# Performance work log

Measured on AMD Instinct MI355X. Metric: run time of the kernel, lower is better.

## Reference

```python
import jax, jax.numpy as jnp
import numpy as np

D_MODEL = 768
N_HEADS = 12
D_K = D_MODEL // N_HEADS
B, S = 4, 2048


def setup_inputs() -> dict:
    key = jax.random.key(0)
    ks = jax.random.split(key, 9)
    sc = 1.0 / np.sqrt(D_MODEL)
    return {
        "query": jax.random.normal(ks[0], (B, S, D_MODEL), jnp.float32),
        "key": jax.random.normal(ks[1], (B, S, D_MODEL), jnp.float32),
        "value": jax.random.normal(ks[2], (B, S, D_MODEL), jnp.float32),
        "W_Q": jax.random.normal(ks[3], (D_MODEL, D_MODEL), jnp.float32) * sc,
        "b_Q": jax.random.normal(ks[4], (D_MODEL,), jnp.float32) * sc,
        "W_K": jax.random.normal(ks[5], (D_MODEL, D_MODEL), jnp.float32) * sc,
        "b_K": jax.random.normal(ks[6], (D_MODEL,), jnp.float32) * sc,
        "W_V": jax.random.normal(ks[7], (D_MODEL, D_MODEL), jnp.float32) * sc,
        "b_V": jax.random.normal(ks[8], (D_MODEL,), jnp.float32) * sc,
    }


def reference(query, key, value, W_Q, b_Q, W_K, b_K, W_V, b_V):
    b = query.shape[0]
    # QKV projections -> [B, H, S, d_k]
    def split_heads(x):
        return x.reshape(b, -1, N_HEADS, D_K).transpose(0, 2, 1, 3)
    q = split_heads(query @ W_Q + b_Q)
    k = split_heads(key @ W_K + b_K)
    v = split_heads(value @ W_V + b_V)
    # scores [B, H, Sq, Sk]
    scores = jnp.einsum("bhqd,bhkd->bhqk", q, k) / np.sqrt(D_K).astype(jnp.float32)
    attn = jax.nn.softmax(scores, axis=-1)
    ctx = jnp.einsum("bhqk,bhkd->bhqd", attn, v)
    # merge heads -> [B, S, d_model]; note: original forward does NOT apply self.linear
    return ctx.transpose(0, 2, 1, 3).reshape(b, -1, N_HEADS * D_K)
```

## Files before the change

### kernel.cpp

```cpp
#include <hip/hip_runtime.h>
#include <math.h>

#define D_MODEL 768
#define NH      12
#define DK      64
#define BATCH   4
#define SEQ     2048
#define QSCALE  0.18033688011112042f
#define MFIX    10.0f

typedef _Float16 v8h __attribute__((ext_vector_type(8)));
typedef _Float16 v4h __attribute__((ext_vector_type(4)));
typedef float    v4f __attribute__((ext_vector_type(4)));
typedef int      v4i __attribute__((ext_vector_type(4)));

#define MFMA16(a, b, c) __builtin_amdgcn_mfma_f32_16x16x32_f16(a, b, c, 0, 0, 0)

__device__ __forceinline__ void async16(const void* g, void* l) {
    __builtin_amdgcn_global_load_lds(
        (const __attribute__((address_space(1))) unsigned int*)g,
        (__attribute__((address_space(3))) unsigned int*)l, 16, 0, 0);
}

#define WH_PER_Z   589824
#define XH_PER_Z   6291456
#define BH_HALVES  131072

__global__ __launch_bounds__(256) void prep_kernel(
    const float* __restrict__ q_in, const float* __restrict__ k_in,
    const float* __restrict__ v_in,
    const float* __restrict__ Wq, const float* __restrict__ Wk,
    const float* __restrict__ Wv,
    _Float16* __restrict__ Xh, _Float16* __restrict__ Wh)
{
    const int kt = blockIdx.x, my = blockIdx.y, z = blockIdx.z;
    const int t = threadIdx.x;
    __shared__ __align__(16) char smraw[32 * 132 * 4];

    if (my < 64) {
        const int mt = my;
        _Float16* Ah = (_Float16*)smraw;
        const float* X = (z == 0) ? q_in : (z == 1) ? k_in : v_in;
        _Float16* dst = Xh + (((size_t)z * 64 + mt) * 24 + kt) * 4096;
        #pragma unroll
        for (int i = 0; i < 4; i++) {
            int f = t + i * 256;
            int m = f >> 3, kq = (f & 7) * 4;
            float4 xv = *(const float4*)&X[((size_t)mt * 128 + m) * D_MODEL +
                                           kt * 32 + kq];
            auto p0 = __builtin_amdgcn_cvt_pkrtz(xv.x, xv.y);
            auto p1 = __builtin_amdgcn_cvt_pkrtz(xv.z, xv.w);
            v4h hv; hv[0] = p0[0]; hv[1] = p0[1]; hv[2] = p1[0]; hv[3] = p1[1];
            *(v4h*)&Ah[((m >> 4) * 64 + (m & 15) + 16 * (kq >> 3)) * 8 + (kq & 7)] = hv;
        }
        __syncthreads();
        #pragma unroll
        for (int it = 0; it < 2; it++) {
            int c = t + it * 256;
            *(v8h*)&dst[c * 8] = *(v8h*)&Ah[c * 8];
        }
    } else {
        float (*Wl)[132] = (float(*)[132])smraw;
        const float* W = (z == 0) ? Wq : (z == 1) ? Wk : Wv;
        const int mtx = my - 64;
        for (int nn = 0; nn < 3; nn++) {
            const int nt = mtx * 3 + nn;
            _Float16* dst = Wh + ((size_t)z * 144 + nt * 24 + kt) * 4096;
            #pragma unroll
            for (int i = 0; i < 4; i++) {
                int f = t + i * 256;
                int r = f >> 5, c4 = (f & 31) * 4;
                *(float4*)&Wl[r][c4] =
                    *(const float4*)&W[(size_t)(kt * 32 + r) * D_MODEL +
                                       nt * 128 + c4];
            }
            __syncthreads();
            #pragma unroll
            for (int it = 0; it < 2; it++) {
                int c = t + it * 256;
                int nsub = c >> 6, cl = c & 63;
                int n = nsub * 16 + (cl & 15);
                int k = (cl >> 4) * 8;
                v8h hv;
                #pragma unroll
                for (int j = 0; j < 8; j++) hv[j] = (_Float16)Wl[k + j][n];
                *(v8h*)&dst[c * 8] = hv;
            }
            __syncthreads();
        }
    }
}

__global__ __launch_bounds__(256) void proj_kernel(
    const _Float16* __restrict__ Xh, const _Float16* __restrict__ Wh,
    const float* __restrict__ bq, const float* __restrict__ bk,
    const float* __restrict__ bv,
    _Float16* __restrict__ Qs, _Float16* __restrict__ Ks,
    _Float16* __restrict__ Vs)
{
    const int d  = blockIdx.x + 6 * (blockIdx.y + 64 * blockIdx.z);
    const int cx = d & 7, jj = d >> 3;
    const int g  = cx + 8 * (jj / 6);
    const int l  = g * 6 + (jj % 6);
    const int nt = l % 6;
    const int mz = l / 6;
    const int mt = mz & 63;
    const int z  = mz >> 6;

    const float* bias = (z == 0) ? bq : (z == 1) ? bk : bv;
    const _Float16* Xz = Xh + ((size_t)z * 64 + mt) * 24 * 4096;
    const _Float16* Wz = Wh + ((size_t)z * 144 + nt * 24) * 4096;

    const int t = threadIdx.x;
    const int lane = t & 63, w = t >> 6;
    const int wm = w & 1, wn = w >> 1;
    const int l15 = lane & 15, quad = lane >> 4;

    __shared__ _Float16 C[128 * 136];

    const _Float16* Abase = Xz + wm * 2048 + lane * 8;
    const _Float16* Bbase = Wz + wn * 2048 + lane * 8;

    v4f acc[4][4];
    #pragma unroll
    for (int i = 0; i < 4; i++)
        #pragma unroll
        for (int j = 0; j < 4; j++) acc[i][j] = (v4f){0.f, 0.f, 0.f, 0.f};

    v8h a[4], b[4];
    #pragma unroll
    for (int i = 0; i < 4; i++) a[i] = *(const v8h*)(Abase + i * 512);
    #pragma unroll
    for (int j = 0; j < 4; j++) b[j] = *(const v8h*)(Bbase + j * 512);

    #pragma unroll 4
    for (int kt = 0; kt < 24; kt++) {
        v8h an[4], bn[4];
        if (kt < 23) {
            const _Float16* An = Abase + (size_t)(kt + 1) * 4096;
            const _Float16* Bn = Bbase + (size_t)(kt + 1) * 4096;
            #pragma unroll
            for (int i = 0; i < 4; i++) an[i] = *(const v8h*)(An + i * 512);
            #pragma unroll
            for (int j = 0; j < 4; j++) bn[j] = *(const v8h*)(Bn + j * 512);
        }
        #pragma unroll
        for (int i = 0; i < 4; i++)
            #pragma unroll
            for (int j = 0; j < 4; j++)
                acc[i][j] = MFMA16(a[i], b[j], acc[i][j]);
        #pragma unroll
        for (int i = 0; i < 4; i++) { a[i] = an[i]; b[i] = bn[i]; }
    }

    if (z < 2) {
        #pragma unroll
        for (int i = 0; i < 4; i++) {
            #pragma unroll
            for (int j = 0; j < 4; j++) {
                float bval = bias[nt * 128 + wn * 64 + j * 16 + l15];
                #pragma unroll
                for (int r = 0; r < 4; r++) {
                    float val = acc[i][j][r] + bval;
                    if (z == 0) val *= QSCALE;
                    C[(wm * 64 + i * 16 + quad * 4 + r) * 136 +
                      wn * 64 + j * 16 + l15] = (_Float16)val;
                }
            }
        }
    } else {
        #pragma unroll
        for (int i = 0; i < 4; i++) {
            #pragma unroll
            for (int j = 0; j < 4; j++) {
                float bval = bias[nt * 128 + wn * 64 + j * 16 + l15];
                v4h hv;
                #pragma unroll
                for (int r = 0; r < 4; r++) hv[r] = (_Float16)(acc[i][j][r] + bval);
                *(v4h*)&C[(wn * 64 + j * 16 + l15) * 136 +
                          wm * 64 + i * 16 + quad * 4] = hv;
            }
        }
    }
    __syncthreads();

    const int bb = mt >> 4;
    if (z < 2) {
        _Float16* dstT = (z == 0) ? Qs : Ks;
        #pragma unroll
        for (int it = 0; it < 8; it++) {
            int c = t + it * 256;
            int hh = c >> 10, cl = c & 1023;
            int qsub = cl >> 7, rest = cl & 127;
            int dt = rest >> 6, cc = rest & 63;
            v8h val = *(v8h*)&C[(qsub * 16 + (cc & 15)) * 136 +
                                hh * 64 + dt * 32 + (cc >> 4) * 8];
            int h = nt * 2 + hh;
            int qt = (mt & 15) * 8 + qsub;
            *(v8h*)&dstT[(size_t)(bb * NH + h) * BH_HALVES +
                         ((qt * 2 + dt) * 64 + cc) * 8] = val;
        }
    } else {
        #pragma unroll
        for (int it = 0; it < 8; it++) {
            int c = t + it * 256;
            int hh = c >> 10, cl = c & 1023;
            int j32s = cl >> 8, rest = cl & 255;
            int dt16 = rest >> 6, cc = rest & 63;
            int gg = cc >> 4, d15 = cc & 15;
            const _Float16* bp =
                &C[(hh * 64 + dt16 * 16 + d15) * 136 + j32s * 32 + gg * 4];
            v4h lo = *(const v4h*)bp;
            v4h hi = *(const v4h*)(bp + 16);
            v8h val;
            val[0] = lo[0]; val[1] = lo[1]; val[2] = lo[2]; val[3] = lo[3];
            val[4] = hi[0]; val[5] = hi[1]; val[6] = hi[2]; val[7] = hi[3];
            int h = nt * 2 + hh;
            int j32g = (mt & 15) * 4 + j32s;
            *(v8h*)&Vs[(size_t)(bb * NH + h) * BH_HALVES +
                       ((j32g * 4 + dt16) * 64 + cc) * 8] = val;
        }
    }
}

__global__ __launch_bounds__(256) void attn_kernel(
    const _Float16* __restrict__ Qs, const _Float16* __restrict__ Ks,
    const _Float16* __restrict__ Vs, float* __restrict__ out)
{
    const int qb = blockIdx.x, h = blockIdx.y, b = blockIdx.z;
    const int t = threadIdx.x;
    const int lane = t & 63, w = t >> 6;
    const int l15 = lane & 15, quad = lane >> 4;
    const size_t bh = (size_t)(b * NH + h);
    const _Float16* Qb = Qs + bh * BH_HALVES;
    const _Float16* Kb = Ks + bh * BH_HALVES;
    const _Float16* Vb = Vs + bh * BH_HALVES;

    __shared__ _Float16 smem[16384];
    _Float16* Kbuf = smem;
    _Float16* Vbuf = smem + 8192;

    v8h qf[2][2];
    #pragma unroll
    for (int i = 0; i < 2; i++)
        #pragma unroll
        for (int dk = 0; dk < 2; dk++) {
            int qt = qb * 8 + w * 2 + i;
            qf[i][dk] = *(const v8h*)&Qb[((qt * 2 + dk) * 64 + lane) * 8];
        }

    v8h ones;
    #pragma unroll
    for (int j = 0; j < 8; j++) ones[j] = (_Float16)1.0f;

    v4f o[2][4];
    v4f osum[2];
    #pragma unroll
    for (int i = 0; i < 2; i++) {
        osum[i] = (v4f){0.f, 0.f, 0.f, 0.f};
        #pragma unroll
        for (int dt = 0; dt < 4; dt++) o[i][dt] = (v4f){0.f, 0.f, 0.f, 0.f};
    }

    auto chunk_compute = [&](const _Float16* Kl, const _Float16* Vl) {
        v4f sc[2][4];
        #pragma unroll
        for (int i = 0; i < 2; i++)
            #pragma unroll
            for (int nt = 0; nt < 4; nt++)
                sc[i][nt] = (v4f){-MFIX, -MFIX, -MFIX, -MFIX};
        __builtin_amdgcn_s_setprio(1);
        #pragma unroll
        for (int nt = 0; nt < 4; nt++) {
            #pragma unroll
            for (int dk = 0; dk < 2; dk++) {
                v8h kf = *(v8h*)&Kl[((nt * 2 + dk) * 64 + lane) * 8];
                sc[0][nt] = MFMA16(kf, qf[0][dk], sc[0][nt]);
                sc[1][nt] = MFMA16(kf, qf[1][dk], sc[1][nt]);
            }
        }
        __builtin_amdgcn_s_setprio(0);

        v4i paw[2][2];
        #pragma unroll
        for (int i = 0; i < 2; i++) {
            #pragma unroll
            for (int nt = 0; nt < 4; nt++) {
                float p0 = __builtin_amdgcn_exp2f(sc[i][nt][0]);
                float p1 = __builtin_amdgcn_exp2f(sc[i][nt][1]);
                float p2 = __builtin_amdgcn_exp2f(sc[i][nt][2]);
                float p3 = __builtin_amdgcn_exp2f(sc[i][nt][3]);
                auto h0 = __builtin_amdgcn_cvt_pkrtz(p0, p1);
                auto h1 = __builtin_amdgcn_cvt_pkrtz(p2, p3);
                paw[i][nt >> 1][(nt & 1) * 2 + 0] = __builtin_bit_cast(int, h0);
                paw[i][nt >> 1][(nt & 1) * 2 + 1] = __builtin_bit_cast(int, h1);
            }
        }

        __builtin_amdgcn_s_setprio(1);
        #pragma unroll
        for (int mf = 0; mf < 2; mf++) {
            v8h pa0 = __builtin_bit_cast(v8h, paw[0][mf]);
            v8h pa1 = __builtin_bit_cast(v8h, paw[1][mf]);
            #pragma unroll
            for (int dt = 0; dt < 4; dt++) {
                v8h vf = *(v8h*)&Vl[((mf * 4 + dt) * 64 + lane) * 8];
                o[0][dt] = MFMA16(pa0, vf, o[0][dt]);
                o[1][dt] = MFMA16(pa1, vf, o[1][dt]);
            }
            osum[0] = MFMA16(pa0, ones, osum[0]);
            osum[1] = MFMA16(pa1, ones, osum[1]);
        }
        __builtin_amdgcn_s_setprio(0);
    };

    async16(Kb + (size_t)t * 8,         Kbuf + t * 8);
    async16(Kb + (size_t)(t + 256) * 8, Kbuf + (t + 256) * 8);
    async16(Vb + (size_t)t * 8,         Vbuf + t * 8);
    async16(Vb + (size_t)(t + 256) * 8, Vbuf + (t + 256) * 8);

    for (int c = 0; c < 32; c += 2) {
        asm volatile("s_waitcnt vmcnt(0)" ::: "memory");
        __syncthreads();
        {
            const _Float16* ks = Kb + (size_t)(c + 1) * 4096;
            const _Float16* vs = Vb + (size_t)(c + 1) * 4096;
            async16(ks + (size_t)t * 8,         Kbuf + 4096 + t * 8);
            async16(ks + (size_t)(t + 256) * 8, Kbuf + 4096 + (t + 256) * 8);
            async16(vs + (size_t)t * 8,         Vbuf + 4096 + t * 8);
            async16(vs + (size_t)(t + 256) * 8, Vbuf + 4096 + (t + 256) * 8);
        }
        chunk_compute(Kbuf, Vbuf);

        asm volatile("s_waitcnt vmcnt(0)" ::: "memory");
        __syncthreads();
        if (c < 30) {
            const _Float16* ks = Kb + (size_t)(c + 2) * 4096;
            const _Float16* vs = Vb + (size_t)(c + 2) * 4096;
            async16(ks + (size_t)t * 8,         Kbuf + t * 8);
            async16(ks + (size_t)(t + 256) * 8, Kbuf + (t + 256) * 8);
            async16(vs + (size_t)t * 8,         Vbuf + t * 8);
            async16(vs + (size_t)(t + 256) * 8, Vbuf + (t + 256) * 8);
        }
        chunk_compute(Kbuf + 4096, Vbuf + 4096);
    }

    #pragma unroll
    for (int i = 0; i < 2; i++) {
        #pragma unroll
        for (int r = 0; r < 4; r++) {
            float inv = 1.0f / osum[i][r];
            int s = qb * 128 + w * 32 + i * 16 + quad * 4 + r;
            #pragma unroll
            for (int dt = 0; dt < 4; dt++)
                out[((size_t)b * SEQ + s) * D_MODEL + h * DK + dt * 16 + l15] =
                    o[i][dt][r] * inv;
        }
    }
}

extern "C" void kernel_launch(void* const* d_in, const int* in_sizes, int n_in,
                              void* d_out, int out_size, void* d_ws, size_t ws_size,
                              hipStream_t stream)
{
    const float* q_in = (const float*)d_in[0];
    const float* k_in = (const float*)d_in[1];
    const float* v_in = (const float*)d_in[2];
    const float* Wq   = (const float*)d_in[3];
    const float* bq   = (const float*)d_in[4];
    const float* Wk   = (const float*)d_in[5];
    const float* bk   = (const float*)d_in[6];
    const float* Wv   = (const float*)d_in[7];
    const float* bv   = (const float*)d_in[8];
    float* out = (float*)d_out;

    _Float16* Wh = (_Float16*)d_ws;
    _Float16* Xh = Wh + 3 * (size_t)WH_PER_Z;
    _Float16* Qs = Xh + 3 * (size_t)XH_PER_Z;
    _Float16* Ks = Qs + (size_t)BATCH * NH * BH_HALVES;
    _Float16* Vs = Ks + (size_t)BATCH * NH * BH_HALVES;

    prep_kernel<<<dim3(24, 66, 3), 256, 0, stream>>>(q_in, k_in, v_in,
                                                     Wq, Wk, Wv, Xh, Wh);
    proj_kernel<<<dim3(6, 64, 3), 256, 0, stream>>>(Xh, Wh, bq, bk, bv,
                                                    Qs, Ks, Vs);
    attn_kernel<<<dim3(16, NH, BATCH), 256, 0, stream>>>(Qs, Ks, Vs, out);
}
```

Before: 240.3 us.

## Fuse fp32-to-fp16 activation conversion into projection GEMM, drop Xh staging

The projection kernel now reads the fp32 query/key/value activations directly and converts them to fp16 in registers right before the MFMAs. The prep pass that wrote a pre-swizzled fp16 copy of the activations is gone, leaving a small kernel that only swizzles the weights. This removes a full write and reread of the 3x8M-element activation buffer and shrinks the prep launch. In exchange, the GEMM loads twice as many bytes per A tile with strided per-row float4 loads, and each block re-reads its activations for every N tile. The loop unroll also drops to 2 to limit register pressure.

After: 300.6 us. +25.1%, slower.

```diff
diff --git a/kernel.cpp b/kernel.cpp
--- a/kernel.cpp
+++ b/kernel.cpp
@@ -23,76 +23,42 @@
 }
 
 #define WH_PER_Z   589824
-#define XH_PER_Z   6291456
 #define BH_HALVES  131072
 
-__global__ __launch_bounds__(256) void prep_kernel(
+__global__ __launch_bounds__(256) void wswz_kernel(
+    const float* __restrict__ Wq, const float* __restrict__ Wk,
+    const float* __restrict__ Wv, _Float16* __restrict__ Wh)
+{
+    const int kt = blockIdx.x, nt = blockIdx.y, z = blockIdx.z;
+    const float* W = (z == 0) ? Wq : (z == 1) ? Wk : Wv;
+    _Float16* dst = Wh + ((size_t)z * 144 + nt * 24 + kt) * 4096;
+    const int t = threadIdx.x;
+
+    __shared__ float Wl[32][132];
+    #pragma unroll
+    for (int i = 0; i < 4; i++) {
+        int f = t + i * 256;
+        int r = f >> 5, c4 = (f & 31) * 4;
+        *(float4*)&Wl[r][c4] =
+            *(const float4*)&W[(size_t)(kt * 32 + r) * D_MODEL + nt * 128 + c4];
+    }
+    __syncthreads();
+    #pragma unroll
+    for (int it = 0; it < 2; it++) {
+        int c = t + it * 256;
+        int nsub = c >> 6, cl = c & 63;
+        int n = nsub * 16 + (cl & 15);
+        int k = (cl >> 4) * 8;
+        v8h hv;
+        #pragma unroll
+        for (int j = 0; j < 8; j++) hv[j] = (_Float16)Wl[k + j][n];
+        *(v8h*)&dst[c * 8] = hv;
+    }
+}
+
+__global__ __launch_bounds__(256) void proj_kernel(
     const float* __restrict__ q_in, const float* __restrict__ k_in,
-    const float* __restrict__ v_in,
-    const float* __restrict__ Wq, const float* __restrict__ Wk,
-    const float* __restrict__ Wv,
-    _Float16* __restrict__ Xh, _Float16* __restrict__ Wh)
-{
-    const int kt = blockIdx.x, my = blockIdx.y, z = blockIdx.z;
-    const int t = threadIdx.x;
-    __shared__ __align__(16) char smraw[32 * 132 * 4];
-
-    if (my < 64) {
-        const int mt = my;
-        _Float16* Ah = (_Float16*)smraw;
-        const float* X = (z == 0) ? q_in : (z == 1) ? k_in : v_in;
-        _Float16* dst = Xh + (((size_t)z * 64 + mt) * 24 + kt) * 4096;
-        #pragma unroll
-        for (int i = 0; i < 4; i++) {
-            int f = t + i * 256;
-            int m = f >> 3, kq = (f & 7) * 4;
-            float4 xv = *(const float4*)&X[((size_t)mt * 128 + m) * D_MODEL +
-                                           kt * 32 + kq];
-            auto p0 = __builtin_amdgcn_cvt_pkrtz(xv.x, xv.y);
-            auto p1 = __builtin_amdgcn_cvt_pkrtz(xv.z, xv.w);
-            v4h hv; hv[0] = p0[0]; hv[1] = p0[1]; hv[2] = p1[0]; hv[3] = p1[1];
-            *(v4h*)&Ah[((m >> 4) * 64 + (m & 15) + 16 * (kq >> 3)) * 8 + (kq & 7)] = hv;
-        }
-        __syncthreads();
-        #pragma unroll
-        for (int it = 0; it < 2; it++) {
-            int c = t + it * 256;
-            *(v8h*)&dst[c * 8] = *(v8h*)&Ah[c * 8];
-        }
-    } else {
-        float (*Wl)[132] = (float(*)[132])smraw;
-        const float* W = (z == 0) ? Wq : (z == 1) ? Wk : Wv;
-        const int mtx = my - 64;
-        for (int nn = 0; nn < 3; nn++) {
-            const int nt = mtx * 3 + nn;
-            _Float16* dst = Wh + ((size_t)z * 144 + nt * 24 + kt) * 4096;
-            #pragma unroll
-            for (int i = 0; i < 4; i++) {
-                int f = t + i * 256;
-                int r = f >> 5, c4 = (f & 31) * 4;
-                *(float4*)&Wl[r][c4] =
-                    *(const float4*)&W[(size_t)(kt * 32 + r) * D_MODEL +
-                                       nt * 128 + c4];
-            }
-            __syncthreads();
-            #pragma unroll
-            for (int it = 0; it < 2; it++) {
-                int c = t + it * 256;
-                int nsub = c >> 6, cl = c & 63;
-                int n = nsub * 16 + (cl & 15);
-                int k = (cl >> 4) * 8;
-                v8h hv;
-                #pragma unroll
-                for (int j = 0; j < 8; j++) hv[j] = (_Float16)Wl[k + j][n];
-                *(v8h*)&dst[c * 8] = hv;
-            }
-            __syncthreads();
-        }
-    }
-}
-
-__global__ __launch_bounds__(256) void proj_kernel(
-    const _Float16* __restrict__ Xh, const _Float16* __restrict__ Wh,
+    const float* __restrict__ v_in, const _Float16* __restrict__ Wh,
     const float* __restrict__ bq, const float* __restrict__ bk,
     const float* __restrict__ bv,
     _Float16* __restrict__ Qs, _Float16* __restrict__ Ks,
@@ -107,8 +73,8 @@
     const int mt = mz & 63;
     const int z  = mz >> 6;
 
+    const float* Xf   = (z == 0) ? q_in : (z == 1) ? k_in : v_in;
     const float* bias = (z == 0) ? bq : (z == 1) ? bk : bv;
-    const _Float16* Xz = Xh + ((size_t)z * 64 + mt) * 24 * 4096;
     const _Float16* Wz = Wh + ((size_t)z * 144 + nt * 24) * 4096;
 
     const int t = threadIdx.x;
@@ -118,7 +84,11 @@
 
     __shared__ _Float16 C[128 * 136];
 
-    const _Float16* Abase = Xz + wm * 2048 + lane * 8;
+    const float* xa[4];
+    #pragma unroll
+    for (int i = 0; i < 4; i++)
+        xa[i] = Xf + (size_t)(mt * 128 + wm * 64 + i * 16 + l15) * D_MODEL +
+                quad * 8;
     const _Float16* Bbase = Wz + wn * 2048 + lane * 8;
 
     v4f acc[4][4];
@@ -127,22 +97,39 @@
         #pragma unroll
         for (int j = 0; j < 4; j++) acc[i][j] = (v4f){0.f, 0.f, 0.f, 0.f};
 
-    v8h a[4], b[4];
-    #pragma unroll
-    for (int i = 0; i < 4; i++) a[i] = *(const v8h*)(Abase + i * 512);
+    float4 af0[4], af1[4];
+    v8h b[4];
+    #pragma unroll
+    for (int i = 0; i < 4; i++) {
+        af0[i] = *(const float4*)&xa[i][0];
+        af1[i] = *(const float4*)&xa[i][4];
+    }
     #pragma unroll
     for (int j = 0; j < 4; j++) b[j] = *(const v8h*)(Bbase + j * 512);
 
-    #pragma unroll 4
+    #pragma unroll 2
     for (int kt = 0; kt < 24; kt++) {
-        v8h an[4], bn[4];
+        float4 an0[4], an1[4];
+        v8h bn[4];
         if (kt < 23) {
-            const _Float16* An = Abase + (size_t)(kt + 1) * 4096;
+            #pragma unroll
+            for (int i = 0; i < 4; i++) {
+                an0[i] = *(const float4*)&xa[i][(kt + 1) * 32];
+                an1[i] = *(const float4*)&xa[i][(kt + 1) * 32 + 4];
+            }
             const _Float16* Bn = Bbase + (size_t)(kt + 1) * 4096;
             #pragma unroll
-            for (int i = 0; i < 4; i++) an[i] = *(const v8h*)(An + i * 512);
-            #pragma unroll
             for (int j = 0; j < 4; j++) bn[j] = *(const v8h*)(Bn + j * 512);
+        }
+        v8h a[4];
+        #pragma unroll
+        for (int i = 0; i < 4; i++) {
+            v4i wds;
+            wds[0] = __builtin_bit_cast(int, __builtin_amdgcn_cvt_pkrtz(af0[i].x, af0[i].y));
+            wds[1] = __builtin_bit_cast(int, __builtin_amdgcn_cvt_pkrtz(af0[i].z, af0[i].w));
+            wds[2] = __builtin_bit_cast(int, __builtin_amdgcn_cvt_pkrtz(af1[i].x, af1[i].y));
+            wds[3] = __builtin_bit_cast(int, __builtin_amdgcn_cvt_pkrtz(af1[i].z, af1[i].w));
+            a[i] = __builtin_bit_cast(v8h, wds);
         }
         #pragma unroll
         for (int i = 0; i < 4; i++)
@@ -150,7 +137,9 @@
             for (int j = 0; j < 4; j++)
                 acc[i][j] = MFMA16(a[i], b[j], acc[i][j]);
         #pragma unroll
-        for (int i = 0; i < 4; i++) { a[i] = an[i]; b[i] = bn[i]; }
+        for (int i = 0; i < 4; i++) {
+            af0[i] = an0[i]; af1[i] = an1[i]; b[i] = bn[i];
+        }
     }
 
     if (z < 2) {
@@ -375,14 +364,12 @@
     float* out = (float*)d_out;
 
     _Float16* Wh = (_Float16*)d_ws;
-    _Float16* Xh = Wh + 3 * (size_t)WH_PER_Z;
-    _Float16* Qs = Xh + 3 * (size_t)XH_PER_Z;
+    _Float16* Qs = Wh + 3 * (size_t)WH_PER_Z;
     _Float16* Ks = Qs + (size_t)BATCH * NH * BH_HALVES;
     _Float16* Vs = Ks + (size_t)BATCH * NH * BH_HALVES;
 
-    prep_kernel<<<dim3(24, 66, 3), 256, 0, stream>>>(q_in, k_in, v_in,
-                                                     Wq, Wk, Wv, Xh, Wh);
-    proj_kernel<<<dim3(6, 64, 3), 256, 0, stream>>>(Xh, Wh, bq, bk, bv,
-                                                    Qs, Ks, Vs);
+    wswz_kernel<<<dim3(24, 6, 3), 256, 0, stream>>>(Wq, Wk, Wv, Wh);
+    proj_kernel<<<dim3(6, 64, 3), 256, 0, stream>>>(q_in, k_in, v_in, Wh,
+                                                    bq, bk, bv, Qs, Ks, Vs);
     attn_kernel<<<dim3(16, NH, BATCH), 256, 0, stream>>>(Qs, Ks, Vs, out);
 }
```
